# Optimization experiments

Hardware: AMD Instinct MI355X
Metric: run time of the kernel (lower is better)

## Reference

```python
import jax, jax.numpy as jnp
import numpy as np

N = 10000       # nodes
E = 640000      # edges
D_IN = 128
D_OUT = 128
EPS = 1e-5      # LayerNorm eps (torch default)


def setup_inputs() -> dict:
    key = jax.random.key(0)
    k_x, k_e, k_w, k_b, k_g = jax.random.split(key, 5)
    x = jax.random.normal(k_x, (N, D_IN), dtype=jnp.float32)
    edge_index = jax.random.randint(k_e, (2, E), 0, N, dtype=jnp.int64)
    # GCNConv linear weight (PyG uses glorot) and bias
    lim = float(np.sqrt(6.0 / (D_IN + D_OUT)))
    W = jax.random.uniform(k_w, (D_IN, D_OUT), minval=-lim, maxval=lim, dtype=jnp.float32)
    b = jnp.zeros((D_OUT,), dtype=jnp.float32)
    # LayerNorm affine params
    gamma = jnp.ones((D_OUT,), dtype=jnp.float32)
    beta = jnp.zeros((D_OUT,), dtype=jnp.float32)
    return {"x": x, "edge_index": edge_index, "W": W, "b": b, "gamma": gamma, "beta": beta}


def reference(x, edge_index, W, b, gamma, beta):
    # --- GCNConv: A_hat = D^{-1/2} (A + I) D^{-1/2}; out = A_hat X W + b ---
    self_idx = jnp.arange(N, dtype=edge_index.dtype)
    src = jnp.concatenate([edge_index[0], self_idx])  # [E+N]
    dst = jnp.concatenate([edge_index[1], self_idx])  # [E+N]
    deg = jax.ops.segment_sum(jnp.ones_like(src, dtype=x.dtype), dst, num_segments=N)
    dinv = jnp.where(deg > 0, jax.lax.rsqrt(deg), 0.0)  # [N]
    norm = dinv[src] * dinv[dst]                        # [E+N]
    h = x @ W                                           # [N, D_OUT] transform first (cheaper)
    msg = h[src] * norm[:, None]                        # [E+N, D_OUT]
    out = jax.ops.segment_sum(msg, dst, num_segments=N) + b
    # --- LayerNorm over feature dim ---
    mu = jnp.mean(out, axis=-1, keepdims=True)
    var = jnp.mean(jnp.square(out - mu), axis=-1, keepdims=True)
    out = (out - mu) * jax.lax.rsqrt(var + EPS) * gamma + beta
    # act = Identity (last_act=ReLU is truthy -> Identity branch); dropout = eval identity; residual=False
    return out
```

## Files before the change

kernel.cpp:

```cpp
#include <hip/hip_runtime.h>
#include <hip/hip_fp16.h>

#define D 128
#define LN_EPS 1e-5f


static __device__ __forceinline__ float h2f(unsigned short h) {
    return __half2float(__builtin_bit_cast(__half, h));
}
static __device__ __forceinline__ unsigned short f2h(float f) {
    return __builtin_bit_cast(unsigned short, __float2half_rn(f));
}

static __device__ __forceinline__ void flagbar(int* slots, int c, int C, int phase) {
    __syncthreads();
    int val = 0x5A5A0001 + phase;
    int tid = threadIdx.x;
    if (tid == 0)
        __hip_atomic_store(&slots[phase * 64 + c], val, __ATOMIC_RELEASE, __HIP_MEMORY_SCOPE_AGENT);
    if (tid < C) {
        while (__hip_atomic_load(&slots[phase * 64 + tid], __ATOMIC_ACQUIRE, __HIP_MEMORY_SCOPE_AGENT) != val)
            __builtin_amdgcn_s_sleep(1);
    }
    __syncthreads();
}

static __device__ __forceinline__ void waitphase(int* slots, int C, int phase) {
    int val = 0x5A5A0001 + phase;
    int tid = threadIdx.x;
    if (tid < C) {
        while (__hip_atomic_load(&slots[phase * 64 + tid], __ATOMIC_ACQUIRE, __HIP_MEMORY_SCOPE_AGENT) != val)
            __builtin_amdgcn_s_sleep(1);
    }
    __syncthreads();
}

#define GMAXR 8

__global__ __launch_bounds__(1024) void build_gemm_kernel(
        const int* __restrict__ src, const int* __restrict__ dst,
        const float* __restrict__ x, const float* __restrict__ W,
        unsigned int* __restrict__ Hh,
        unsigned short* __restrict__ ghist, int* __restrict__ blocksum,
        int* __restrict__ rowptr, float* __restrict__ dinv,
        unsigned short* __restrict__ csr, int* __restrict__ bar,
        int N, int E, int Ec, int C, int G) {
    extern __shared__ int lds[];
    __shared__ int s_scan[20];
    int c = blockIdx.x;
    int tid = threadIdx.x;
    int lane = tid & 63, wv = tid >> 6;

    if (c >= C) {
        unsigned int* sWh = (unsigned int*)lds;
        #pragma unroll
        for (int i = tid; i < D * D / 2; i += 1024) {
            float2 v = ((const float2*)W)[i];
            sWh[i] = (unsigned int)f2h(v.x) | ((unsigned int)f2h(v.y) << 16);
        }
        __syncthreads();
        int gb = c - C;
        int nb = G - C;
        int nper = (N + nb - 1) / nb;
        int r0 = gb * nper;
        int rn = min(nper, N - r0); if (rn < 0) rn = 0;

        float2 acc[GMAXR];
        #pragma unroll
        for (int j = 0; j < GMAXR; j++) {
            acc[j] = make_float2(0.f, 0.f);
            int lr = wv + 16 * j;
            if (lr < rn) {
                float2 xr = ((const float2*)x)[(size_t)(r0 + lr) * 64 + lane];
                float y0 = 0.f, y1 = 0.f;
                #pragma unroll 8
                for (int k = 0; k < 64; k++) {
                    float g0 = __shfl(xr.x, k);
                    float g1 = __shfl(xr.y, k);
                    unsigned int w0 = sWh[(2 * k) * 64 + lane];
                    unsigned int w1 = sWh[(2 * k + 1) * 64 + lane];
                    y0 += g0 * h2f((unsigned short)w0) + g1 * h2f((unsigned short)w1);
                    y1 += g0 * h2f((unsigned short)(w0 >> 16)) + g1 * h2f((unsigned short)(w1 >> 16));
                }
                acc[j] = make_float2(y0, y1);
            }
        }
        waitphase(bar, C, 1);
        #pragma unroll
        for (int j = 0; j < GMAXR; j++) {
            int lr = wv + 16 * j;
            if (lr < rn) {
                float dr = dinv[r0 + lr];
                Hh[(size_t)(r0 + lr) * 64 + lane] =
                    (unsigned int)f2h(acc[j].x * dr) | ((unsigned int)f2h(acc[j].y * dr) << 16);
            }
        }
        return;
    }

    for (int i = tid; i < N; i += 1024) lds[i] = 0;
    __syncthreads();
    int lo = c * Ec, hi = min(lo + Ec, E);
    #pragma unroll 4
    for (int i = lo + tid; i < hi; i += 1024)
        atomicAdd(&lds[dst[i]], 1);
    __syncthreads();
    for (int i = tid; i < N; i += 1024)
        ghist[(size_t)c * N + i] = (unsigned short)lds[i];
    flagbar(bar, c, C, 0);

    int nper = (N + C - 1) / C;
    int n0 = c * nper;
    int nn = min(nper, N - n0); if (nn < 0) nn = 0;
    int mydeg = 0;
    if (tid < nn) {
        int n = n0 + tid;
        int run = 0;
        #pragma unroll 8
        for (int cc = 0; cc < C; cc++) {
            int t = ghist[(size_t)cc * N + n];
            ghist[(size_t)cc * N + n] = (unsigned short)run;
            run += t;
        }
        mydeg = run;
        dinv[n] = rsqrtf((float)(run + 1));
    }
    int incl = mydeg;
    #pragma unroll
    for (int off = 1; off < 64; off <<= 1) {
        int y = __shfl_up(incl, off);
        if (lane >= off) incl += y;
    }
    if (lane == 63) s_scan[wv] = incl;
    __syncthreads();
    if (tid == 0) {
        int run = 0;
        #pragma unroll
        for (int k = 0; k < 16; k++) { int t = s_scan[k]; s_scan[k] = run; run += t; }
        blocksum[c] = run;
    }
    __syncthreads();
    if (tid < nn) rowptr[n0 + tid] = s_scan[wv] + incl - mydeg;
    flagbar(bar, c, C, 1);

    if (tid < 64) {
        int bs = (tid < C) ? blocksum[tid] : 0;
        int inc2 = bs;
        #pragma unroll
        for (int off = 1; off < 64; off <<= 1) {
            int y = __shfl_up(inc2, off);
            if (tid >= off) inc2 += y;
        }
        if (tid == c)     s_scan[18] = inc2 - bs;
        if (tid == C - 1) s_scan[19] = inc2;
    }
    __syncthreads();
    int base = s_scan[18];
    if (tid < nn) rowptr[n0 + tid] += base;
    if (c == C - 1 && tid == 0) rowptr[N] = s_scan[19];
    flagbar(bar, c, C, 2);

    for (int i = tid; i < N; i += 1024)
        lds[i] = rowptr[i] + ghist[(size_t)c * N + i];
    __syncthreads();
    #pragma unroll 4
    for (int i = lo + tid; i < hi; i += 1024) {
        int d = dst[i];
        int pos = atomicAdd(&lds[d], 1);
        csr[pos] = (unsigned short)src[i];
    }
}

__global__ __launch_bounds__(512) void fused_agg(const unsigned int* __restrict__ Hh,
                                                 const int* __restrict__ rowptr,
                                                 const unsigned short* __restrict__ csr,
                                                 const float* __restrict__ dinv,
                                                 const float* __restrict__ bias,
                                                 const float* __restrict__ gamma,
                                                 const float* __restrict__ beta,
                                                 float* __restrict__ out, int N) {
    int w = threadIdx.x >> 6, lane = threadIdx.x & 63;
    int node = blockIdx.x * 8 + w;
    if (node >= N) return;
    float dn = dinv[node];

    unsigned int hv0 = Hh[node * 64 + lane];
    float a0 = h2f((unsigned short)hv0);
    float a1 = h2f((unsigned short)(hv0 >> 16));

    int start = rowptr[node], end = rowptr[node + 1];
    int base = start;
    for (; base + 64 <= end; base += 64) {
        int s = csr[base + lane];
        #pragma unroll 8
        for (int k = 0; k < 64; k++) {
            int sk = __shfl(s, k);
            unsigned int hv = Hh[sk * 64 + lane];
            a0 += h2f((unsigned short)hv);
            a1 += h2f((unsigned short)(hv >> 16));
        }
    }
    int rem = end - base;
    if (rem > 0) {
        int s = 0;
        if (lane < rem) s = csr[base + lane];
        for (int k = 0; k < rem; k++) {
            int sk = __shfl(s, k);
            unsigned int hv = Hh[sk * 64 + lane];
            a0 += h2f((unsigned short)hv);
            a1 += h2f((unsigned short)(hv >> 16));
        }
    }

    int c0 = lane * 2;
    float y0 = dn * a0 + bias[c0];
    float y1 = dn * a1 + bias[c0 + 1];

    float sum = y0 + y1, sq = y0 * y0 + y1 * y1;
    #pragma unroll
    for (int off = 32; off > 0; off >>= 1) {
        sum += __shfl_xor(sum, off);
        sq  += __shfl_xor(sq, off);
    }
    float mean = sum * (1.0f / D);
    float var  = sq * (1.0f / D) - mean * mean;
    float inv  = rsqrtf(var + LN_EPS);
    float o0 = (y0 - mean) * inv * gamma[c0] + beta[c0];
    float o1 = (y1 - mean) * inv * gamma[c0 + 1] + beta[c0 + 1];
    *(float2*)(out + (size_t)node * D + c0) = make_float2(o0, o1);
}


__global__ void deg_kernel(const int* __restrict__ dst, int* __restrict__ deg, int E) {
    int e = blockIdx.x * blockDim.x + threadIdx.x;
    if (e < E) atomicAdd(&deg[dst[e]], 1);
}
__global__ __launch_bounds__(1024) void scan_kernel(const int* __restrict__ deg,
                                                    int* __restrict__ rowptr,
                                                    int* __restrict__ fill,
                                                    float* __restrict__ dinv, int N) {
    __shared__ int s_wsum[16];
    __shared__ int s_woff[16];
    __shared__ int s_carry;
    int t = threadIdx.x;
    int lane = t & 63, w = t >> 6;
    if (t == 0) s_carry = 0;
    __syncthreads();
    for (int base = 0; base < N; base += 1024) {
        int i = base + t;
        int v = (i < N) ? deg[i] : 0;
        int incl = v;
        #pragma unroll
        for (int off = 1; off < 64; off <<= 1) {
            int y = __shfl_up(incl, off);
            if (lane >= off) incl += y;
        }
        if (lane == 63) s_wsum[w] = incl;
        __syncthreads();
        if (t == 0) {
            int run = s_carry;
            #pragma unroll
            for (int k = 0; k < 16; k++) { s_woff[k] = run; run += s_wsum[k]; }
            s_carry = run;
        }
        __syncthreads();
        if (i < N) {
            int rp = s_woff[w] + (incl - v);
            rowptr[i] = rp;
            fill[i] = rp;
            dinv[i] = rsqrtf((float)(v + 1));
        }
    }
    if (t == 0) rowptr[N] = s_carry;
}
__global__ void fill_kernel(const int* __restrict__ src, const int* __restrict__ dst,
                            int* __restrict__ fill, unsigned short* __restrict__ csr, int E) {
    int e = blockIdx.x * blockDim.x + threadIdx.x;
    if (e < E) {
        int pos = atomicAdd(&fill[dst[e]], 1);
        csr[pos] = (unsigned short)src[e];
    }
}
__global__ __launch_bounds__(512) void fused_fp32(const float* __restrict__ x,
                                                  const float* __restrict__ W,
                                                  const int* __restrict__ rowptr,
                                                  const unsigned short* __restrict__ csr,
                                                  const float* __restrict__ dinv,
                                                  const float* __restrict__ bias,
                                                  const float* __restrict__ gamma,
                                                  const float* __restrict__ beta,
                                                  float* __restrict__ out, int N) {
    __shared__ float sW[D * D];
    {
        const float4* Wv = (const float4*)W;
        float4* sWv = (float4*)sW;
        #pragma unroll
        for (int i = 0; i < (D * D / 4) / 512; i++)
            sWv[threadIdx.x + i * 512] = Wv[threadIdx.x + i * 512];
    }
    __syncthreads();
    int w = threadIdx.x >> 6, lane = threadIdx.x & 63;
    int node = blockIdx.x * 8 + w;
    if (node >= N) return;
    float dn = dinv[node];
    int c0 = lane * 2;
    float2 xv = *(const float2*)(x + (size_t)node * D + c0);
    float a0 = xv.x * dn * dn, a1 = xv.y * dn * dn;
    int start = rowptr[node], end = rowptr[node + 1];
    int base = start;
    for (; base + 64 <= end; base += 64) {
        int s = csr[base + lane];
        float wt = dinv[s] * dn;
        #pragma unroll 8
        for (int k = 0; k < 64; k++) {
            int sk = __shfl(s, k);
            float wk = __shfl(wt, k);
            float2 xs = *(const float2*)(x + (size_t)sk * D + c0);
            a0 += xs.x * wk; a1 += xs.y * wk;
        }
    }
    int rem = end - base;
    if (rem > 0) {
        int s = 0; float wt = 0.f;
        if (lane < rem) { s = csr[base + lane]; wt = dinv[s] * dn; }
        for (int k = 0; k < rem; k++) {
            int sk = __shfl(s, k);
            float wk = __shfl(wt, k);
            float2 xs = *(const float2*)(x + (size_t)sk * D + c0);
            a0 += xs.x * wk; a1 += xs.y * wk;
        }
    }
    float y0 = bias[c0], y1 = bias[c0 + 1];
    #pragma unroll 8
    for (int k = 0; k < 64; k++) {
        float g0 = __shfl(a0, k);
        float g1 = __shfl(a1, k);
        float2 w0 = *(const float2*)(sW + (2 * k) * D + c0);
        float2 w1 = *(const float2*)(sW + (2 * k + 1) * D + c0);
        y0 += g0 * w0.x + g1 * w1.x;
        y1 += g0 * w0.y + g1 * w1.y;
    }
    float sum = y0 + y1, sq = y0 * y0 + y1 * y1;
    #pragma unroll
    for (int off = 32; off > 0; off >>= 1) {
        sum += __shfl_xor(sum, off);
        sq  += __shfl_xor(sq, off);
    }
    float mean = sum * (1.0f / D);
    float var  = sq * (1.0f / D) - mean * mean;
    float inv  = rsqrtf(var + LN_EPS);
    float o0 = (y0 - mean) * inv * gamma[c0] + beta[c0];
    float o1 = (y1 - mean) * inv * gamma[c0 + 1] + beta[c0 + 1];
    *(float2*)(out + (size_t)node * D + c0) = make_float2(o0, o1);
}

extern "C" void kernel_launch(void* const* d_in, const int* in_sizes, int n_in,
                              void* d_out, int out_size, void* d_ws, size_t ws_size,
                              hipStream_t stream) {
    const float* x     = (const float*)d_in[0];
    const int*   ei    = (const int*)d_in[1];
    const float* W     = (const float*)d_in[2];
    const float* bias  = (const float*)d_in[3];
    const float* gamma = (const float*)d_in[4];
    const float* beta  = (const float*)d_in[5];
    float*       out   = (float*)d_out;

    int N = in_sizes[0] / D;
    int E = in_sizes[1] / 2;
    const int* src = ei;
    const int* dst = ei + E;

    char* ws = (char*)d_ws;
    size_t off = 0;
    auto carve = [&](size_t bytes) { size_t p = off; off = (off + bytes + 15) & ~15UL; return (void*)(ws + p); };
    int*            bar      = (int*)           carve(3 * 64 * 4);
    int*            blocksum = (int*)           carve(64 * 4);
    int*            rowptr   = (int*)           carve((size_t)(N + 1) * 4);
    float*          dinv     = (float*)         carve((size_t)N * 4);
    unsigned short* csr      = (unsigned short*)carve((size_t)E * 2);
    unsigned int*   Hh       = (unsigned int*)  carve((size_t)N * (D / 2) * 4);
    size_t fixed_end = off;

    int C = 0;
    if (ws_size > fixed_end + 16) {
        size_t avail = ws_size - fixed_end - 16;
        size_t cmax = avail / ((size_t)N * 2);
        C = (int)((cmax > 64) ? 64 : cmax);
    }

    const int G = 256;
    bool gemm_ok = (C >= 16) && ((size_t)(G - C) * 16 * GMAXR >= (size_t)N);

    if (gemm_ok) {
        unsigned short* ghist = (unsigned short*)carve((size_t)C * N * 2);
        int Ec = (E + C - 1) / C;
        size_t lds = (size_t)N * 4;
        if (lds < (size_t)(D * D / 2) * 4) lds = (size_t)(D * D / 2) * 4;
        build_gemm_kernel<<<G, 1024, lds, stream>>>(src, dst, x, W, Hh, ghist,
                                                    blocksum, rowptr, dinv, csr,
                                                    bar, N, E, Ec, C, G);
        fused_agg<<<(N + 7) / 8, 512, 0, stream>>>(Hh, rowptr, csr, dinv,
                                                   bias, gamma, beta, out, N);
    } else {
        int* deg  = (int*)carve((size_t)N * 4);
        int* fill = (int*)carve((size_t)N * 4);
        hipMemsetAsync(deg, 0, (size_t)N * 4, stream);
        deg_kernel<<<(E + 255) / 256, 256, 0, stream>>>(dst, deg, E);
        scan_kernel<<<1, 1024, 0, stream>>>(deg, rowptr, fill, dinv, N);
        fill_kernel<<<(E + 255) / 256, 256, 0, stream>>>(src, dst, fill, csr, E);
        fused_fp32<<<(N + 7) / 8, 512, 0, stream>>>(x, W, rowptr, csr, dinv,
                                                    bias, gamma, beta, out, N);
    }
}
```

Baseline: 142.4 us.

## Fuse aggregation and LayerNorm into persistent build/GEMM kernel via grid barrier

Merges the separate aggregation kernel into the persistent build+GEMM kernel, adding a grid-wide done barrier over all 256 blocks, after which every wave handles nodes in a grid-stride loop. The GEMM blocks now store unscaled H and no longer wait for dinv. The aggregation instead multiplies each gathered neighbour row by the source dinv, loaded once per 64-edge chunk and broadcast by shuffle. This removes a kernel launch and the GEMM blocks' wait on the scan phase. In exchange it adds a per-edge multiply, relies on all 256 blocks being co-resident, and leaves aggregation with only 256x16 waves.

```diff
diff --git a/kernel.cpp b/kernel.cpp
--- a/kernel.cpp
+++ b/kernel.cpp
@@ -25,25 +25,31 @@
     __syncthreads();
 }
 
-static __device__ __forceinline__ void waitphase(int* slots, int C, int phase) {
-    int val = 0x5A5A0001 + phase;
+static __device__ __forceinline__ void donebar(int* slots, int c, int G) {
+    __syncthreads();
+    const int val = 0x5A5A000A;
     int tid = threadIdx.x;
-    if (tid < C) {
-        while (__hip_atomic_load(&slots[phase * 64 + tid], __ATOMIC_ACQUIRE, __HIP_MEMORY_SCOPE_AGENT) != val)
-            __builtin_amdgcn_s_sleep(1);
+    if (tid == 0)
+        __hip_atomic_store(&slots[c], val, __ATOMIC_RELEASE, __HIP_MEMORY_SCOPE_AGENT);
+    if (tid < G) {
+        while (__hip_atomic_load(&slots[tid], __ATOMIC_ACQUIRE, __HIP_MEMORY_SCOPE_AGENT) != val)
+            __builtin_amdgcn_s_sleep(16);
     }
     __syncthreads();
 }
 
 #define GMAXR 8
 
-__global__ __launch_bounds__(1024) void build_gemm_kernel(
+__global__ __launch_bounds__(1024) void mega_kernel(
         const int* __restrict__ src, const int* __restrict__ dst,
         const float* __restrict__ x, const float* __restrict__ W,
         unsigned int* __restrict__ Hh,
         unsigned short* __restrict__ ghist, int* __restrict__ blocksum,
         int* __restrict__ rowptr, float* __restrict__ dinv,
         unsigned short* __restrict__ csr, int* __restrict__ bar,
+        int* __restrict__ done,
+        const float* __restrict__ bias, const float* __restrict__ gamma,
+        const float* __restrict__ beta, float* __restrict__ out,
         int N, int E, int Ec, int C, int G) {
     extern __shared__ int lds[];
     __shared__ int s_scan[20];
@@ -65,10 +71,8 @@
         int r0 = gb * nper;
         int rn = min(nper, N - r0); if (rn < 0) rn = 0;
 
-        float2 acc[GMAXR];
         #pragma unroll
         for (int j = 0; j < GMAXR; j++) {
-            acc[j] = make_float2(0.f, 0.f);
             int lr = wv + 16 * j;
             if (lr < rn) {
                 float2 xr = ((const float2*)x)[(size_t)(r0 + lr) * 64 + lane];
@@ -82,152 +86,138 @@
                     y0 += g0 * h2f((unsigned short)w0) + g1 * h2f((unsigned short)w1);
                     y1 += g0 * h2f((unsigned short)(w0 >> 16)) + g1 * h2f((unsigned short)(w1 >> 16));
                 }
-                acc[j] = make_float2(y0, y1);
+                Hh[(size_t)(r0 + lr) * 64 + lane] =
+                    (unsigned int)f2h(y0) | ((unsigned int)f2h(y1) << 16);
             }
         }
-        waitphase(bar, C, 1);
-        #pragma unroll
-        for (int j = 0; j < GMAXR; j++) {
-            int lr = wv + 16 * j;
-            if (lr < rn) {
-                float dr = dinv[r0 + lr];
-                Hh[(size_t)(r0 + lr) * 64 + lane] =
-                    (unsigned int)f2h(acc[j].x * dr) | ((unsigned int)f2h(acc[j].y * dr) << 16);
+    } else {
+        for (int i = tid; i < N; i += 1024) lds[i] = 0;
+        __syncthreads();
+        int lo = c * Ec, hi = min(lo + Ec, E);
+        #pragma unroll 4
+        for (int i = lo + tid; i < hi; i += 1024)
+            atomicAdd(&lds[dst[i]], 1);
+        __syncthreads();
+        for (int i = tid; i < N; i += 1024)
+            ghist[(size_t)c * N + i] = (unsigned short)lds[i];
+        flagbar(bar, c, C, 0);
+
+        int nper = (N + C - 1) / C;
+        int n0 = c * nper;
+        int nn = min(nper, N - n0); if (nn < 0) nn = 0;
+        int mydeg = 0;
+        if (tid < nn) {
+            int n = n0 + tid;
+            int run = 0;
+            #pragma unroll 8
+            for (int cc = 0; cc < C; cc++) {
+                int t = ghist[(size_t)cc * N + n];
+                ghist[(size_t)cc * N + n] = (unsigned short)run;
+                run += t;
             }
-        }
-        return;
-    }
-
-    for (int i = tid; i < N; i += 1024) lds[i] = 0;
-    __syncthreads();
-    int lo = c * Ec, hi = min(lo + Ec, E);
-    #pragma unroll 4
-    for (int i = lo + tid; i < hi; i += 1024)
-        atomicAdd(&lds[dst[i]], 1);
-    __syncthreads();
-    for (int i = tid; i < N; i += 1024)
-        ghist[(size_t)c * N + i] = (unsigned short)lds[i];
-    flagbar(bar, c, C, 0);
-
-    int nper = (N + C - 1) / C;
-    int n0 = c * nper;
-    int nn = min(nper, N - n0); if (nn < 0) nn = 0;
-    int mydeg = 0;
-    if (tid < nn) {
-        int n = n0 + tid;
-        int run = 0;
-        #pragma unroll 8
-        for (int cc = 0; cc < C; cc++) {
-            int t = ghist[(size_t)cc * N + n];
-            ghist[(size_t)cc * N + n] = (unsigned short)run;
-            run += t;
-        }
-        mydeg = run;
-        dinv[n] = rsqrtf((float)(run + 1));
-    }
-    int incl = mydeg;
-    #pragma unroll
-    for (int off = 1; off < 64; off <<= 1) {
-        int y = __shfl_up(incl, off);
-        if (lane >= off) incl += y;
-    }
-    if (lane == 63) s_scan[wv] = incl;
-    __syncthreads();
-    if (tid == 0) {
-        int run = 0;
-        #pragma unroll
-        for (int k = 0; k < 16; k++) { int t = s_scan[k]; s_scan[k] = run; run += t; }
-        blocksum[c] = run;
-    }
-    __syncthreads();
-    if (tid < nn) rowptr[n0 + tid] = s_scan[wv] + incl - mydeg;
-    flagbar(bar, c, C, 1);
-
-    if (tid < 64) {
-        int bs = (tid < C) ? blocksum[tid] : 0;
-        int inc2 = bs;
+            mydeg = run;
+            dinv[n] = rsqrtf((float)(run + 1));
+        }
+        int incl = mydeg;
         #pragma unroll
         for (int off = 1; off < 64; off <<= 1) {
-            int y = __shfl_up(inc2, off);
-            if (tid >= off) inc2 += y;
-        }
-        if (tid == c)     s_scan[18] = inc2 - bs;
-        if (tid == C - 1) s_scan[19] = inc2;
-    }
-    __syncthreads();
-    int base = s_scan[18];
-    if (tid < nn) rowptr[n0 + tid] += base;
-    if (c == C - 1 && tid == 0) rowptr[N] = s_scan[19];
-    flagbar(bar, c, C, 2);
-
-    for (int i = tid; i < N; i += 1024)
-        lds[i] = rowptr[i] + ghist[(size_t)c * N + i];
-    __syncthreads();
-    #pragma unroll 4
-    for (int i = lo + tid; i < hi; i += 1024) {
-        int d = dst[i];
-        int pos = atomicAdd(&lds[d], 1);
-        csr[pos] = (unsigned short)src[i];
-    }
-}
-
-__global__ __launch_bounds__(512) void fused_agg(const unsigned int* __restrict__ Hh,
-                                                 const int* __restrict__ rowptr,
-                                                 const unsigned short* __restrict__ csr,
-                                                 const float* __restrict__ dinv,
-                                                 const float* __restrict__ bias,
-                                                 const float* __restrict__ gamma,
-                                                 const float* __restrict__ beta,
-                                                 float* __restrict__ out, int N) {
-    int w = threadIdx.x >> 6, lane = threadIdx.x & 63;
-    int node = blockIdx.x * 8 + w;
-    if (node >= N) return;
-    float dn = dinv[node];
-
-    unsigned int hv0 = Hh[node * 64 + lane];
-    float a0 = h2f((unsigned short)hv0);
-    float a1 = h2f((unsigned short)(hv0 >> 16));
-
-    int start = rowptr[node], end = rowptr[node + 1];
-    int base = start;
-    for (; base + 64 <= end; base += 64) {
-        int s = csr[base + lane];
-        #pragma unroll 8
-        for (int k = 0; k < 64; k++) {
-            int sk = __shfl(s, k);
-            unsigned int hv = Hh[sk * 64 + lane];
-            a0 += h2f((unsigned short)hv);
-            a1 += h2f((unsigned short)(hv >> 16));
-        }
-    }
-    int rem = end - base;
-    if (rem > 0) {
-        int s = 0;
-        if (lane < rem) s = csr[base + lane];
-        for (int k = 0; k < rem; k++) {
-            int sk = __shfl(s, k);
-            unsigned int hv = Hh[sk * 64 + lane];
-            a0 += h2f((unsigned short)hv);
-            a1 += h2f((unsigned short)(hv >> 16));
-        }
-    }
-
+            int y = __shfl_up(incl, off);
+            if (lane >= off) incl += y;
+        }
+        if (lane == 63) s_scan[wv] = incl;
+        __syncthreads();
+        if (tid == 0) {
+            int run = 0;
+            #pragma unroll
+            for (int k = 0; k < 16; k++) { int t = s_scan[k]; s_scan[k] = run; run += t; }
+            blocksum[c] = run;
+        }
+        __syncthreads();
+        if (tid < nn) rowptr[n0 + tid] = s_scan[wv] + incl - mydeg;
+        flagbar(bar, c, C, 1);
+
+        if (tid < 64) {
+            int bs = (tid < C) ? blocksum[tid] : 0;
+            int inc2 = bs;
+            #pragma unroll
+            for (int off = 1; off < 64; off <<= 1) {
+                int y = __shfl_up(inc2, off);
+                if (tid >= off) inc2 += y;
+            }
+            if (tid == c)     s_scan[18] = inc2 - bs;
+            if (tid == C - 1) s_scan[19] = inc2;
+        }
+        __syncthreads();
+        int base = s_scan[18];
+        if (tid < nn) rowptr[n0 + tid] += base;
+        if (c == C - 1 && tid == 0) rowptr[N] = s_scan[19];
+        flagbar(bar, c, C, 2);
+
+        for (int i = tid; i < N; i += 1024)
+            lds[i] = rowptr[i] + ghist[(size_t)c * N + i];
+        __syncthreads();
+        #pragma unroll 4
+        for (int i = lo + tid; i < hi; i += 1024) {
+            int d = dst[i];
+            int pos = atomicAdd(&lds[d], 1);
+            csr[pos] = (unsigned short)src[i];
+        }
+    }
+
+    donebar(done, c, G);
+
+    int wid = c * 16 + wv;
+    int nwv = G * 16;
     int c0 = lane * 2;
-    float y0 = dn * a0 + bias[c0];
-    float y1 = dn * a1 + bias[c0 + 1];
-
-    float sum = y0 + y1, sq = y0 * y0 + y1 * y1;
-    #pragma unroll
-    for (int off = 32; off > 0; off >>= 1) {
-        sum += __shfl_xor(sum, off);
-        sq  += __shfl_xor(sq, off);
-    }
-    float mean = sum * (1.0f / D);
-    float var  = sq * (1.0f / D) - mean * mean;
-    float inv  = rsqrtf(var + LN_EPS);
-    float o0 = (y0 - mean) * inv * gamma[c0] + beta[c0];
-    float o1 = (y1 - mean) * inv * gamma[c0 + 1] + beta[c0 + 1];
-    *(float2*)(out + (size_t)node * D + c0) = make_float2(o0, o1);
+    for (int node = wid; node < N; node += nwv) {
+        float dn = dinv[node];
+        unsigned int hv0 = Hh[(size_t)node * 64 + lane];
+        float a0 = h2f((unsigned short)hv0) * dn;
+        float a1 = h2f((unsigned short)(hv0 >> 16)) * dn;
+
+        int start = rowptr[node], end = rowptr[node + 1];
+        int base = start;
+        for (; base + 64 <= end; base += 64) {
+            int s = csr[base + lane];
+            float wt = dinv[s];
+            #pragma unroll 8
+            for (int k = 0; k < 64; k++) {
+                int sk = __shfl(s, k);
+                float wk = __shfl(wt, k);
+                unsigned int hv = Hh[(size_t)sk * 64 + lane];
+                a0 += h2f((unsigned short)hv) * wk;
+                a1 += h2f((unsigned short)(hv >> 16)) * wk;
+            }
+        }
+        int rem = end - base;
+        if (rem > 0) {
+            int s = 0; float wt = 0.f;
+            if (lane < rem) { s = csr[base + lane]; wt = dinv[s]; }
+            for (int k = 0; k < rem; k++) {
+                int sk = __shfl(s, k);
+                float wk = __shfl(wt, k);
+                unsigned int hv = Hh[(size_t)sk * 64 + lane];
+                a0 += h2f((unsigned short)hv) * wk;
+                a1 += h2f((unsigned short)(hv >> 16)) * wk;
+            }
+        }
+
+        float y0 = dn * a0 + bias[c0];
+        float y1 = dn * a1 + bias[c0 + 1];
+
+        float sum = y0 + y1, sq = y0 * y0 + y1 * y1;
+        #pragma unroll
+        for (int off = 32; off > 0; off >>= 1) {
+            sum += __shfl_xor(sum, off);
+            sq  += __shfl_xor(sq, off);
+        }
+        float mean = sum * (1.0f / D);
+        float var  = sq * (1.0f / D) - mean * mean;
+        float inv  = rsqrtf(var + LN_EPS);
+        float o0 = (y0 - mean) * inv * gamma[c0] + beta[c0];
+        float o1 = (y1 - mean) * inv * gamma[c0 + 1] + beta[c0 + 1];
+        *(float2*)(out + (size_t)node * D + c0) = make_float2(o0, o1);
+    }
 }
 
 
@@ -374,6 +364,7 @@
     size_t off = 0;
     auto carve = [&](size_t bytes) { size_t p = off; off = (off + bytes + 15) & ~15UL; return (void*)(ws + p); };
     int*            bar      = (int*)           carve(3 * 64 * 4);
+    int*            done     = (int*)           carve(256 * 4);
     int*            blocksum = (int*)           carve(64 * 4);
     int*            rowptr   = (int*)           carve((size_t)(N + 1) * 4);
     float*          dinv     = (float*)         carve((size_t)N * 4);
@@ -389,18 +380,17 @@
     }
 
     const int G = 256;
-    bool gemm_ok = (C >= 16) && ((size_t)(G - C) * 16 * GMAXR >= (size_t)N);
-
-    if (gemm_ok) {
+    bool ok = (C >= 16) && ((size_t)(G - C) * 16 * GMAXR >= (size_t)N) && (N <= 60000);
+
+    if (ok) {
         unsigned short* ghist = (unsigned short*)carve((size_t)C * N * 2);
         int Ec = (E + C - 1) / C;
         size_t lds = (size_t)N * 4;
         if (lds < (size_t)(D * D / 2) * 4) lds = (size_t)(D * D / 2) * 4;
-        build_gemm_kernel<<<G, 1024, lds, stream>>>(src, dst, x, W, Hh, ghist,
-                                                    blocksum, rowptr, dinv, csr,
-                                                    bar, N, E, Ec, C, G);
-        fused_agg<<<(N + 7) / 8, 512, 0, stream>>>(Hh, rowptr, csr, dinv,
-                                                   bias, gamma, beta, out, N);
+        mega_kernel<<<G, 1024, lds, stream>>>(src, dst, x, W, Hh, ghist,
+                                              blocksum, rowptr, dinv, csr,
+                                              bar, done, bias, gamma, beta,
+                                              out, N, E, Ec, C, G);
     } else {
         int* deg  = (int*)carve((size_t)N * 4);
         int* fill = (int*)carve((size_t)N * 4);
```

Result: slower. 246.3 us (+73.0%).
